# Optimization experiments

Measured on AMD Instinct MI355X. Metric: run time of the kernel, lower is better.

## Reference

```python
import jax, jax.numpy as jnp
import numpy as np

N_IND, N_COM, N_TRU = 100000, 100000, 100000
N = N_IND + N_COM + N_TRU
E = 4800000
H = 64
NUM_CLASSES = 2


def _sage(x, src, dst, Wl, Wr, b):
    # PyG SAGEConv (mean aggr): out = lin_l(mean_{j in N(i)} x_j) + lin_r(x_i)
    msg = x[src]                                   # [E, H] gather
    agg = jax.ops.segment_sum(msg, dst, num_segments=N)           # [N, H]
    cnt = jax.ops.segment_sum(jnp.ones((src.shape[0],), x.dtype), dst, num_segments=N)
    mean = agg / jnp.maximum(cnt, 1.0)[:, None]
    return mean @ Wl + x @ Wr + b


def setup_inputs() -> dict:
    key = jax.random.key(0)
    ks = jax.random.split(key, 20)
    inp = {
        "x_individual": jax.random.normal(ks[0], (N_IND, 32), jnp.float32),
        "x_company": jax.random.normal(ks[1], (N_COM, 48), jnp.float32),
        "x_trust": jax.random.normal(ks[2], (N_TRU, 24), jnp.float32),
        "edge_index": jax.random.randint(ks[3], (2, E), 0, N, jnp.int64 if jax.config.jax_enable_x64 else jnp.int32),
    }
    def lin(k, fan_in, fan_out):
        s = 1.0 / np.sqrt(fan_in)
        return jax.random.uniform(k, (fan_in, fan_out), jnp.float32, -s, s)
    inp.update({
        "W_ind": lin(ks[4], 32, H), "b_ind": jnp.zeros((H,), jnp.float32),
        "W_com": lin(ks[5], 48, H), "b_com": jnp.zeros((H,), jnp.float32),
        "W_tru": lin(ks[6], 24, H), "b_tru": jnp.zeros((H,), jnp.float32),
        "W1l": lin(ks[7], H, H), "W1r": lin(ks[8], H, H), "b1": jnp.zeros((H,), jnp.float32),
        "W2l": lin(ks[9], H, H), "W2r": lin(ks[10], H, H), "b2": jnp.zeros((H,), jnp.float32),
        "Wc1": lin(ks[11], H, H // 2), "bc1": jnp.zeros((H // 2,), jnp.float32),
        "Wc2": lin(ks[12], H // 2, NUM_CLASSES), "bc2": jnp.zeros((NUM_CLASSES,), jnp.float32),
    })
    return inp


def reference(x_individual, x_company, x_trust, edge_index,
              W_ind, b_ind, W_com, b_com, W_tru, b_tru,
              W1l, W1r, b1, W2l, W2r, b2, Wc1, bc1, Wc2, bc2):
    # per-type linear encoders, then concat along node dim
    x = jnp.concatenate([
        x_individual @ W_ind + b_ind,
        x_company @ W_com + b_com,
        x_trust @ W_tru + b_tru,
    ], axis=0)  # [N, H]
    src, dst = edge_index[0], edge_index[1]
    x = jax.nn.relu(_sage(x, src, dst, W1l, W1r, b1))
    x = jax.nn.relu(_sage(x, src, dst, W2l, W2r, b2))
    # classifier MLP (dropout is identity in eval mode)
    h = jax.nn.relu(x @ Wc1 + bc1)
    return h @ Wc2 + bc2  # [N, num_classes]
```

## Files before the change

### kernel.cpp

```cpp
#include <hip/hip_runtime.h>

#define N_IND 100000
#define N_COM 100000
#define N_TRU 100000
#define NTOT  300000
#define NEDGE 4800000
#define HDIM  64
#define CHUNK 8192
#define NCHUNKS 586
#define NCB 293
#define CAP 18432
#define PADW 33
#define NTILES32 9375
#define NBLK_ENC1 391
#define NBLK_ENC  1173
#define NBLK_MEGA 1759

typedef float v4f __attribute__((ext_vector_type(4)));
typedef unsigned short v4u __attribute__((ext_vector_type(4)));
typedef unsigned short v8u __attribute__((ext_vector_type(8)));
typedef _Float16 v8h __attribute__((ext_vector_type(8)));

static __device__ __forceinline__ float elem4(const float4 v, int j) {
  return j == 0 ? v.x : j == 1 ? v.y : j == 2 ? v.z : v.w;
}

static __device__ __forceinline__ unsigned short f2h(float f) {
  _Float16 h = (_Float16)f;
  return __builtin_bit_cast(unsigned short, h);
}
static __device__ __forceinline__ float h2f(unsigned short u) {
  return (float)__builtin_bit_cast(_Float16, u);
}

static __device__ __forceinline__ void fmix2(float& alo, float& ahi, unsigned pk) {
  asm("v_fma_mix_f32 %0, %1, 1.0, %0 op_sel:[0,0,0] op_sel_hi:[1,0,0]"
      : "+v"(alo) : "v"(pk));
  asm("v_fma_mix_f32 %0, %1, 1.0, %0 op_sel:[1,0,0] op_sel_hi:[1,0,0]"
      : "+v"(ahi) : "v"(pk));
}

static __device__ __forceinline__ void store_rows_f16(
    unsigned short* __restrict__ out, float* __restrict__ st, const float* acc,
    int node0, int rows, int tid, bool active) {
#pragma unroll
  for (int stage = 0; stage < 2; ++stage) {
    __syncthreads();
    if (active) {
#pragma unroll
      for (int j = 0; j < 32; ++j) st[tid * PADW + j] = acc[stage * 32 + j];
    }
    __syncthreads();
#pragma unroll
    for (int it = 0; it < 8; ++it) {
      int e = it * 256 + tid;
      int r = e >> 3;
      int c = (e & 7) * 4;
      if (r < rows) {
        v4u o;
        o.x = f2h(st[r * PADW + c + 0]);
        o.y = f2h(st[r * PADW + c + 1]);
        o.z = f2h(st[r * PADW + c + 2]);
        o.w = f2h(st[r * PADW + c + 3]);
        *(v4u*)(out + (size_t)(node0 + r) * HDIM + stage * 32 + c) = o;
      }
    }
  }
}

template <int K>
static __device__ void encode_body(
    const float* __restrict__ xin, const float* __restrict__ W,
    const float* __restrict__ b, unsigned short* __restrict__ xhout,
    int n, int base, int blk, float* st) {
  int tid = threadIdx.x;
  int node0 = blk * 256;
  int node = node0 + tid;
  bool active = node < n;
  int rows = min(256, n - node0);
  float acc[HDIM];
  if (active) {
    float4 row[K / 4];
    const float4* xv = (const float4*)(xin + (size_t)node * K);
#pragma unroll
    for (int i = 0; i < K / 4; ++i) row[i] = xv[i];
#pragma unroll
    for (int f = 0; f < HDIM; ++f) acc[f] = b[f];
#pragma unroll
    for (int k4 = 0; k4 < K / 4; ++k4) {
#pragma unroll
      for (int j = 0; j < 4; ++j) {
        float xs = elem4(row[k4], j);
        int k = k4 * 4 + j;
#pragma unroll
        for (int f = 0; f < HDIM; ++f) acc[f] += xs * W[k * HDIM + f];
      }
    }
  }
  store_rows_f16(xhout + (size_t)base * HDIM, st, acc, node0, rows, tid, active);
}

static __device__ void scatter_body(
    const int* __restrict__ src, const int* __restrict__ dst,
    int* __restrict__ ccur, unsigned* __restrict__ packed, int e, int blk,
    char* smem) {
  int* h = (int*)smem;
  int* gofs = h + NCB;
  int* sv = gofs + NCB;
  unsigned* vals = (unsigned*)(sv + 512);
  unsigned short* sbid = (unsigned short*)(vals + CHUNK);
  int tid = threadIdx.x;
  int start = blk * CHUNK;
  int len = min(CHUNK, e - start);

  for (int i = tid; i < NCB; i += 256) h[i] = 0;
  __syncthreads();

  int dreg[CHUNK / 256];
#pragma unroll
  for (int k = 0; k < CHUNK / 256; ++k) {
    int i = k * 256 + tid;
    dreg[k] = (i < len) ? dst[start + i] : -1;
    if (i < len) atomicAdd(&h[dreg[k] >> 10], 1);
  }
  __syncthreads();

  sv[tid] = (tid < NCB) ? h[tid] : 0;
  sv[tid + 256] = (tid + 256 < NCB) ? h[tid + 256] : 0;
  __syncthreads();
  for (int o = 1; o < 512; o <<= 1) {
    int y0 = (tid >= o) ? sv[tid - o] : 0;
    int y1 = sv[tid + 256 - o];
    __syncthreads();
    sv[tid] += y0;
    sv[tid + 256] += y1;
    __syncthreads();
  }
  for (int b = tid; b < NCB; b += 256) {
    int c = h[b];
    int lo = (b == 0) ? 0 : sv[b - 1];
    int gb = (c > 0) ? atomicAdd(&ccur[b], c) : 0;
    gofs[b] = gb - lo;
    h[b] = lo;
  }
  __syncthreads();

#pragma unroll
  for (int k = 0; k < CHUNK / 256; ++k) {
    int i = k * 256 + tid;
    if (i < len) {
      int d = dreg[k];
      int s = src[start + i];
      int b = d >> 10;
      int slot = atomicAdd(&h[b], 1);
      vals[slot] = ((unsigned)s << 10) | (unsigned)(d & 1023);
      sbid[slot] = (unsigned short)b;
    }
  }
  __syncthreads();

  for (int i = tid; i < len; i += 256) {
    int b = sbid[i];
    packed[gofs[b] + i] = vals[i];
  }
}

__global__ __launch_bounds__(256, 2) void mega_front_kernel(
    const float* __restrict__ x_ind, const float* __restrict__ W_ind, const float* __restrict__ b_ind,
    const float* __restrict__ x_com, const float* __restrict__ W_com, const float* __restrict__ b_com,
    const float* __restrict__ x_tru, const float* __restrict__ W_tru, const float* __restrict__ b_tru,
    unsigned short* __restrict__ xh0,
    const int* __restrict__ src, const int* __restrict__ dst,
    int* __restrict__ ccur, unsigned* __restrict__ packed) {
  __shared__ __align__(16) char smem[53568];
  int bid = blockIdx.x;
  if (bid < NBLK_ENC1) {
    encode_body<32>(x_ind, W_ind, b_ind, xh0, N_IND, 0, bid, (float*)smem);
  } else if (bid < 2 * NBLK_ENC1) {
    encode_body<48>(x_com, W_com, b_com, xh0, N_COM, N_IND, bid - NBLK_ENC1, (float*)smem);
  } else if (bid < NBLK_ENC) {
    encode_body<24>(x_tru, W_tru, b_tru, xh0, N_TRU, N_IND + N_COM, bid - 2 * NBLK_ENC1,
                    (float*)smem);
  } else {
    scatter_body(src, dst, ccur, packed, NEDGE, bid - NBLK_ENC, smem);
  }
}

__global__ __launch_bounds__(256) void prep_weights_kernel(
    const float* __restrict__ W1l, const float* __restrict__ W1r,
    const float* __restrict__ W2l, const float* __restrict__ W2r,
    unsigned short* __restrict__ out, int* __restrict__ ccur) {
  int bid = blockIdx.x;
  int tid = threadIdx.x;
  if (bid == 64) {
    for (int b = tid; b < NCB; b += 256) ccur[b] = b * CAP;
    return;
  }
  int idx = bid * 256 + tid;
  int m = idx >> 12;
  int id2 = idx & 4095;
  const float* W = (m == 0) ? W1l : (m == 1) ? W1r : (m == 2) ? W2l : W2r;
  int j = id2 & 7;
  int l = (id2 >> 3) & 63;
  int ts = id2 >> 9;
  int t = ts >> 1, s = ts & 1;
  int k = s * 32 + (l >> 4) * 8 + j;
  int n = t * 16 + (l & 15);
  out[m * 4096 + id2] = f2h(W[k * HDIM + n]);
}

__global__ __launch_bounds__(1024) void sort_coarse_kernel(
    const unsigned* __restrict__ packed, const int* __restrict__ ccur,
    int* __restrict__ eidx, int* __restrict__ nodeoff, int* __restrict__ deg) {
  __shared__ int cnts[1024];
  __shared__ int cur[1024];
  __shared__ int sv[1024];
  int cb = blockIdx.x;
  int tid = threadIdx.x;
  cnts[tid] = 0;
  __syncthreads();
  int base = cb * CAP;
  int cnt = ccur[cb] - base;
  for (int i = tid; i < cnt; i += 1024)
    atomicAdd(&cnts[packed[base + i] & 1023u], 1);
  __syncthreads();
  int c = cnts[tid];
  sv[tid] = c;
  __syncthreads();
  for (int o = 1; o < 1024; o <<= 1) {
    int y = (tid >= o) ? sv[tid - o] : 0;
    __syncthreads();
    sv[tid] += y;
    __syncthreads();
  }
  int ex = sv[tid] - c;
  cur[tid] = ex;
  int node = (cb << 10) + tid;
  if (node < NTOT) { deg[node] = c; nodeoff[node] = base + ex; }
  __syncthreads();
  for (int i = tid; i < cnt; i += 1024) {
    unsigned pr = packed[base + i];
    int dl = (int)(pr & 1023u);
    int r = atomicAdd(&cur[dl], 1);
    eidx[base + r] = (int)(pr >> 10);
  }
}

#define SMPAD 72
template <bool LAYER2>
__global__ __launch_bounds__(256, 7) void agg_combine_kernel(
    const unsigned short* __restrict__ xh, const int* __restrict__ off,
    const int* __restrict__ deg, const int* __restrict__ eidx,
    const unsigned short* __restrict__ wfrag,
    const float* __restrict__ bb,
    unsigned short* __restrict__ outh,
    const float* __restrict__ Wc1, const float* __restrict__ bc1,
    const float* __restrict__ Wc2, const float* __restrict__ bc2,
    float* __restrict__ dout) {
  __shared__ unsigned short smean[32 * SMPAD];
  __shared__ float st[32 * 68 + 8];
  __shared__ float sW1[LAYER2 ? 2048 : 8];
  int tid = threadIdx.x;
  int node0 = blockIdx.x * 32;

  {
    int nit = tid >> 3;
    int lane8 = tid & 7;
    int node = node0 + nit;
    int start = off[node];
    int d = deg[node];
    const char* xb = (const char*)xh;
    unsigned rofs = (unsigned)(lane8 << 4);
    float acc[16];
#pragma unroll
    for (int j = 0; j < 16; ++j) acc[j] = 0.f;
    int i = 0;
    for (; i + 8 <= d; i += 8) {
      const int* ep = eidx + start + i;
      int s[8];
#pragma unroll
      for (int k = 0; k < 8; ++k) s[k] = ep[k];
      uint4 v[8];
#pragma unroll
      for (int k = 0; k < 8; ++k)
        v[k] = *(const uint4*)(xb + ((((unsigned)s[k]) << 7) + rofs));
#pragma unroll
      for (int k = 0; k < 8; ++k) {
        float* a = &acc[(k & 1) * 8];
        fmix2(a[0], a[1], v[k].x);
        fmix2(a[2], a[3], v[k].y);
        fmix2(a[4], a[5], v[k].z);
        fmix2(a[6], a[7], v[k].w);
      }
    }
    if (i + 4 <= d) {
      const int* ep = eidx + start + i;
      int s[4];
#pragma unroll
      for (int k = 0; k < 4; ++k) s[k] = ep[k];
      uint4 v[4];
#pragma unroll
      for (int k = 0; k < 4; ++k)
        v[k] = *(const uint4*)(xb + ((((unsigned)s[k]) << 7) + rofs));
#pragma unroll
      for (int k = 0; k < 4; ++k) {
        float* a = &acc[(k & 1) * 8];
        fmix2(a[0], a[1], v[k].x);
        fmix2(a[2], a[3], v[k].y);
        fmix2(a[4], a[5], v[k].z);
        fmix2(a[6], a[7], v[k].w);
      }
      i += 4;
    }
    for (; i < d; ++i) {
      int s = eidx[start + i];
      uint4 v = *(const uint4*)(xb + ((((unsigned)s) << 7) + rofs));
      fmix2(acc[0], acc[1], v.x);
      fmix2(acc[2], acc[3], v.y);
      fmix2(acc[4], acc[5], v.z);
      fmix2(acc[6], acc[7], v.w);
    }
    float inv = 1.0f / (float)(d > 0 ? d : 1);
    v8u o;
#pragma unroll
    for (int j = 0; j < 8; ++j) o[j] = f2h((acc[j] + acc[8 + j]) * inv);
    *(v8u*)&smean[nit * SMPAD + lane8 * 8] = o;
  }
  if (LAYER2) {
    for (int i = tid; i < 2048; i += 256) sW1[i] = Wc1[i];
  }
  __syncthreads();

  int wid = tid >> 6;
  int lane = tid & 63;
  int mlo = lane & 15;
  int quad = lane >> 4;
  {
    const v8h* wf = (const v8h*)wfrag;
#pragma unroll
    for (int p = 0; p < 2; ++p) {
      int task = wid * 2 + p;
      int rt = task >> 2, cb = task & 3;
      v8h BL0 = wf[(cb * 2 + 0) * 64 + lane];
      v8h BL1 = wf[(cb * 2 + 1) * 64 + lane];
      v8h BR0 = wf[512 + (cb * 2 + 0) * 64 + lane];
      v8h BR1 = wf[512 + (cb * 2 + 1) * 64 + lane];
      float bias = bb[cb * 16 + mlo];
      int arow = rt * 16 + mlo;
      v8h Am0 = *(const v8h*)&smean[arow * SMPAD + quad * 8];
      v8h Am1 = *(const v8h*)&smean[arow * SMPAD + quad * 8 + 32];
      const _Float16* xrow =
          (const _Float16*)xh + (size_t)(node0 + arow) * HDIM + quad * 8;
      v8h Ax0 = *(const v8h*)(xrow);
      v8h Ax1 = *(const v8h*)(xrow + 32);
      v4f acc = {bias, bias, bias, bias};
      acc = __builtin_amdgcn_mfma_f32_16x16x32_f16(Am0, BL0, acc, 0, 0, 0);
      acc = __builtin_amdgcn_mfma_f32_16x16x32_f16(Am1, BL1, acc, 0, 0, 0);
      acc = __builtin_amdgcn_mfma_f32_16x16x32_f16(Ax0, BR0, acc, 0, 0, 0);
      acc = __builtin_amdgcn_mfma_f32_16x16x32_f16(Ax1, BR1, acc, 0, 0, 0);
#pragma unroll
      for (int r = 0; r < 4; ++r)
        st[(rt * 16 + quad * 4 + r) * 68 + cb * 16 + mlo] = fmaxf(acc[r], 0.f);
    }
  }
  __syncthreads();

  if (!LAYER2) {
    int r = tid >> 3;
    int c = (tid & 7) * 8;
    const float* ap = &st[r * 68 + c];
    v8u o;
#pragma unroll
    for (int j = 0; j < 8; ++j) o[j] = f2h(ap[j]);
    *(v8u*)(outh + (size_t)(node0 + r) * HDIM + c) = o;
  } else {
    int nd = tid >> 3;
    int f = (tid & 7) * 4;
    float h0 = bc1[f], h1 = bc1[f + 1], h2 = bc1[f + 2], h3 = bc1[f + 3];
    const float* xr = &st[nd * 68];
#pragma unroll
    for (int k = 0; k < 64; ++k) {
      float xv = xr[k];
      h0 += xv * sW1[k * 32 + f + 0];
      h1 += xv * sW1[k * 32 + f + 1];
      h2 += xv * sW1[k * 32 + f + 2];
      h3 += xv * sW1[k * 32 + f + 3];
    }
    h0 = fmaxf(h0, 0.f); h1 = fmaxf(h1, 0.f);
    h2 = fmaxf(h2, 0.f); h3 = fmaxf(h3, 0.f);
    float o0 = h0 * Wc2[f * 2 + 0] + h1 * Wc2[(f + 1) * 2 + 0] +
               h2 * Wc2[(f + 2) * 2 + 0] + h3 * Wc2[(f + 3) * 2 + 0];
    float o1 = h0 * Wc2[f * 2 + 1] + h1 * Wc2[(f + 1) * 2 + 1] +
               h2 * Wc2[(f + 2) * 2 + 1] + h3 * Wc2[(f + 3) * 2 + 1];
#pragma unroll
    for (int m = 4; m >= 1; m >>= 1) {
      o0 += __shfl_xor(o0, m);
      o1 += __shfl_xor(o1, m);
    }
    if ((tid & 7) == 0) {
      float2 ov;
      ov.x = o0 + bc2[0];
      ov.y = o1 + bc2[1];
      *(float2*)(dout + (size_t)(node0 + nd) * 2) = ov;
    }
  }
}

extern "C" void kernel_launch(void* const* d_in, const int* in_sizes, int n_in,
                              void* d_out, int out_size, void* d_ws, size_t ws_size,
                              hipStream_t stream) {
  const float* x_ind = (const float*)d_in[0];
  const float* x_com = (const float*)d_in[1];
  const float* x_tru = (const float*)d_in[2];
  const int*   ei    = (const int*)d_in[3];
  const float* W_ind = (const float*)d_in[4];
  const float* b_ind = (const float*)d_in[5];
  const float* W_com = (const float*)d_in[6];
  const float* b_com = (const float*)d_in[7];
  const float* W_tru = (const float*)d_in[8];
  const float* b_tru = (const float*)d_in[9];
  const float* W1l = (const float*)d_in[10];
  const float* W1r = (const float*)d_in[11];
  const float* b1  = (const float*)d_in[12];
  const float* W2l = (const float*)d_in[13];
  const float* W2r = (const float*)d_in[14];
  const float* b2  = (const float*)d_in[15];
  const float* Wc1 = (const float*)d_in[16];
  const float* bc1 = (const float*)d_in[17];
  const float* Wc2 = (const float*)d_in[18];
  const float* bc2 = (const float*)d_in[19];

  const int* srcp = ei;
  const int* dstp = ei + NEDGE;

  size_t fcount = (size_t)NTOT * HDIM;
  size_t pksz = (size_t)NCB * CAP;
  unsigned* packed = (unsigned*)d_ws;
  unsigned short* xh0 = (unsigned short*)(packed + pksz);
  unsigned short* xh1 = xh0 + fcount;
  int* eidx    = (int*)(xh1 + fcount);
  int* nodeoff = eidx + pksz;
  int* deg     = nodeoff + NTOT;
  int* ccur    = deg + NTOT;
  unsigned short* wfrag = (unsigned short*)((((size_t)(ccur + NCB)) + 15) & ~(size_t)15);
  size_t needed = (size_t)((char*)(wfrag + 4 * 4096) - (char*)d_ws) + 64;
  if (ws_size < needed) return;

  prep_weights_kernel<<<65, 256, 0, stream>>>(W1l, W1r, W2l, W2r, wfrag, ccur);

  mega_front_kernel<<<NBLK_MEGA, 256, 0, stream>>>(
      x_ind, W_ind, b_ind, x_com, W_com, b_com, x_tru, W_tru, b_tru,
      xh0, srcp, dstp, ccur, packed);

  sort_coarse_kernel<<<NCB, 1024, 0, stream>>>(packed, ccur, eidx, nodeoff, deg);

  agg_combine_kernel<false><<<NTILES32, 256, 0, stream>>>(
      xh0, nodeoff, deg, eidx, wfrag, b1, xh1, nullptr, nullptr, nullptr, nullptr, nullptr);

  agg_combine_kernel<true><<<NTILES32, 256, 0, stream>>>(
      xh1, nodeoff, deg, eidx, wfrag + 2 * 4096, b2, nullptr, Wc1, bc1, Wc2, bc2,
      (float*)d_out);
}
```

Before: 463.8 us.

## Halve scatter chunk size for higher occupancy; compute degrees via global atomics in scatter

The scatter chunk shrinks from 8192 to 4096 edges, which cuts shared memory per block and raises the launch-bounds occupancy hint from 2 to 4 blocks per CU, with twice as many scatter blocks. Per-node degrees are now counted with global atomicAdd during the scatter (zeroed in the prep kernel), so the sort kernel no longer needs its shared-memory counting pass over the packed edges. The trade is 4.8M extra global atomics to randomly distributed addresses, in exchange for removing one read pass and raising parallelism.

```diff
diff --git a/kernel.cpp b/kernel.cpp
--- a/kernel.cpp
+++ b/kernel.cpp
@@ -6,15 +6,16 @@
 #define NTOT  300000
 #define NEDGE 4800000
 #define HDIM  64
-#define CHUNK 8192
-#define NCHUNKS 586
+#define CHUNK 4096
+#define NCHUNKS_SC 1172
 #define NCB 293
 #define CAP 18432
 #define PADW 33
 #define NTILES32 9375
 #define NBLK_ENC1 391
 #define NBLK_ENC  1173
-#define NBLK_MEGA 1759
+#define NBLK_MEGA 2345
+#define NBLK_PREP 1237
 
 typedef float v4f __attribute__((ext_vector_type(4)));
 typedef unsigned short v4u __attribute__((ext_vector_type(4)));
@@ -102,8 +103,8 @@
 
 static __device__ void scatter_body(
     const int* __restrict__ src, const int* __restrict__ dst,
-    int* __restrict__ ccur, unsigned* __restrict__ packed, int e, int blk,
-    char* smem) {
+    int* __restrict__ ccur, unsigned* __restrict__ packed, int* __restrict__ deg,
+    int e, int blk, char* smem) {
   int* h = (int*)smem;
   int* gofs = h + NCB;
   int* sv = gofs + NCB;
@@ -121,7 +122,10 @@
   for (int k = 0; k < CHUNK / 256; ++k) {
     int i = k * 256 + tid;
     dreg[k] = (i < len) ? dst[start + i] : -1;
-    if (i < len) atomicAdd(&h[dreg[k] >> 10], 1);
+    if (i < len) {
+      atomicAdd(&h[dreg[k] >> 10], 1);
+      atomicAdd(&deg[dreg[k]], 1);
+    }
   }
   __syncthreads();
 
@@ -165,14 +169,14 @@
   }
 }
 
-__global__ __launch_bounds__(256, 2) void mega_front_kernel(
+__global__ __launch_bounds__(256, 4) void mega_front_kernel(
     const float* __restrict__ x_ind, const float* __restrict__ W_ind, const float* __restrict__ b_ind,
     const float* __restrict__ x_com, const float* __restrict__ W_com, const float* __restrict__ b_com,
     const float* __restrict__ x_tru, const float* __restrict__ W_tru, const float* __restrict__ b_tru,
     unsigned short* __restrict__ xh0,
     const int* __restrict__ src, const int* __restrict__ dst,
-    int* __restrict__ ccur, unsigned* __restrict__ packed) {
-  __shared__ __align__(16) char smem[53568];
+    int* __restrict__ ccur, unsigned* __restrict__ packed, int* __restrict__ deg) {
+  __shared__ __align__(16) char smem[33792];
   int bid = blockIdx.x;
   if (bid < NBLK_ENC1) {
     encode_body<32>(x_ind, W_ind, b_ind, xh0, N_IND, 0, bid, (float*)smem);
@@ -182,49 +186,46 @@
     encode_body<24>(x_tru, W_tru, b_tru, xh0, N_TRU, N_IND + N_COM, bid - 2 * NBLK_ENC1,
                     (float*)smem);
   } else {
-    scatter_body(src, dst, ccur, packed, NEDGE, bid - NBLK_ENC, smem);
+    scatter_body(src, dst, ccur, packed, deg, NEDGE, bid - NBLK_ENC, smem);
   }
 }
 
 __global__ __launch_bounds__(256) void prep_weights_kernel(
     const float* __restrict__ W1l, const float* __restrict__ W1r,
     const float* __restrict__ W2l, const float* __restrict__ W2r,
-    unsigned short* __restrict__ out, int* __restrict__ ccur) {
+    unsigned short* __restrict__ out, int* __restrict__ ccur, int* __restrict__ deg) {
   int bid = blockIdx.x;
   int tid = threadIdx.x;
-  if (bid == 64) {
+  if (bid < 64) {
+    int idx = bid * 256 + tid;
+    int m = idx >> 12;
+    int id2 = idx & 4095;
+    const float* W = (m == 0) ? W1l : (m == 1) ? W1r : (m == 2) ? W2l : W2r;
+    int j = id2 & 7;
+    int l = (id2 >> 3) & 63;
+    int ts = id2 >> 9;
+    int t = ts >> 1, s = ts & 1;
+    int k = s * 32 + (l >> 4) * 8 + j;
+    int n = t * 16 + (l & 15);
+    out[m * 4096 + id2] = f2h(W[k * HDIM + n]);
+  } else if (bid == 64) {
     for (int b = tid; b < NCB; b += 256) ccur[b] = b * CAP;
-    return;
-  }
-  int idx = bid * 256 + tid;
-  int m = idx >> 12;
-  int id2 = idx & 4095;
-  const float* W = (m == 0) ? W1l : (m == 1) ? W1r : (m == 2) ? W2l : W2r;
-  int j = id2 & 7;
-  int l = (id2 >> 3) & 63;
-  int ts = id2 >> 9;
-  int t = ts >> 1, s = ts & 1;
-  int k = s * 32 + (l >> 4) * 8 + j;
-  int n = t * 16 + (l & 15);
-  out[m * 4096 + id2] = f2h(W[k * HDIM + n]);
+  } else {
+    int n = (bid - 65) * 256 + tid;
+    if (n < NTOT) deg[n] = 0;
+  }
 }
 
 __global__ __launch_bounds__(1024) void sort_coarse_kernel(
     const unsigned* __restrict__ packed, const int* __restrict__ ccur,
-    int* __restrict__ eidx, int* __restrict__ nodeoff, int* __restrict__ deg) {
-  __shared__ int cnts[1024];
+    const int* __restrict__ deg, int* __restrict__ eidx, int* __restrict__ nodeoff) {
   __shared__ int cur[1024];
   __shared__ int sv[1024];
   int cb = blockIdx.x;
   int tid = threadIdx.x;
-  cnts[tid] = 0;
-  __syncthreads();
+  int node = (cb << 10) + tid;
   int base = cb * CAP;
-  int cnt = ccur[cb] - base;
-  for (int i = tid; i < cnt; i += 1024)
-    atomicAdd(&cnts[packed[base + i] & 1023u], 1);
-  __syncthreads();
-  int c = cnts[tid];
+  int c = (node < NTOT) ? deg[node] : 0;
   sv[tid] = c;
   __syncthreads();
   for (int o = 1; o < 1024; o <<= 1) {
@@ -235,9 +236,9 @@
   }
   int ex = sv[tid] - c;
   cur[tid] = ex;
-  int node = (cb << 10) + tid;
-  if (node < NTOT) { deg[node] = c; nodeoff[node] = base + ex; }
-  __syncthreads();
+  if (node < NTOT) nodeoff[node] = base + ex;
+  __syncthreads();
+  int cnt = ccur[cb] - base;
   for (int i = tid; i < cnt; i += 1024) {
     unsigned pr = packed[base + i];
     int dl = (int)(pr & 1023u);
@@ -446,13 +447,13 @@
   size_t needed = (size_t)((char*)(wfrag + 4 * 4096) - (char*)d_ws) + 64;
   if (ws_size < needed) return;
 
-  prep_weights_kernel<<<65, 256, 0, stream>>>(W1l, W1r, W2l, W2r, wfrag, ccur);
+  prep_weights_kernel<<<NBLK_PREP, 256, 0, stream>>>(W1l, W1r, W2l, W2r, wfrag, ccur, deg);
 
   mega_front_kernel<<<NBLK_MEGA, 256, 0, stream>>>(
       x_ind, W_ind, b_ind, x_com, W_com, b_com, x_tru, W_tru, b_tru,
-      xh0, srcp, dstp, ccur, packed);
-
-  sort_coarse_kernel<<<NCB, 1024, 0, stream>>>(packed, ccur, eidx, nodeoff, deg);
+      xh0, srcp, dstp, ccur, packed, deg);
+
+  sort_coarse_kernel<<<NCB, 1024, 0, stream>>>(packed, ccur, deg, eidx, nodeoff);
 
   agg_combine_kernel<false><<<NTILES32, 256, 0, stream>>>(
       xh0, nodeoff, deg, eidx, wfrag, b1, xh1, nullptr, nullptr, nullptr, nullptr, nullptr);
```

After: 618.4 us. 1.33x slower.
